# Optimization experiments

Measured on AMD Instinct MI355X. Metric: run time of the kernel, lower is better.

## Reference

```python
import jax, jax.numpy as jnp
import numpy as np

B, T, I, H, O = 64, 2048, 128, 256, 128


def setup_inputs() -> dict:
    key = jax.random.key(0)
    ks = jax.random.split(key, 7)
    s_xh = 1.0 / np.sqrt(I)
    s_hh = 1.0 / np.sqrt(H)
    return {
        "x": jax.random.normal(ks[0], (B, T, I), dtype=jnp.float32),
        "h0": jax.random.normal(ks[1], (B, H), dtype=jnp.float32),
        "Wxh": jax.random.uniform(ks[2], (H, I), jnp.float32, -s_xh, s_xh),
        "Whh": jax.random.uniform(ks[3], (H, H), jnp.float32, -s_hh, s_hh),
        "bh": jax.random.uniform(ks[4], (H,), jnp.float32, -s_hh, s_hh),
        "Wout": jax.random.uniform(ks[5], (O, H), jnp.float32, -s_hh, s_hh),
        "bout": jax.random.uniform(ks[6], (O,), jnp.float32, -s_hh, s_hh),
    }


def reference(x, h0, Wxh, Whh, bh, Wout, bout):
    # x: (B, T, I) -> scan over time with hidden state h: (B, H)
    def step(h, xt):
        # Elman cell: h' = tanh(x Wxh^T + h Whh^T + b)
        h_new = jnp.tanh(xt @ Wxh.T + h @ Whh.T + bh)
        y = h_new @ Wout.T + bout  # (B, O) per-step output head
        return h_new, y

    xT = jnp.swapaxes(x, 0, 1)  # (T, B, I)
    hT, Ys = jax.lax.scan(step, h0, xT)
    Y = jnp.swapaxes(Ys, 0, 1)  # (B, T, O)
    return Y, hT
```

## Files before the change

kernel.cpp:

```cpp
#include <hip/hip_runtime.h>
#include <hip/hip_bf16.h>
#include <hip/hip_fp16.h>

#define B_SZ 64
#define T_SZ 2048
#define I_SZ 128
#define H_SZ 256
#define O_SZ 128

typedef _Float16 half_t;
typedef _Float16 h2_t __attribute__((ext_vector_type(2)));
typedef __fp16   fp16x2_t __attribute__((ext_vector_type(2)));
typedef _Float16 h8_t __attribute__((ext_vector_type(8)));
typedef float    f4_t __attribute__((ext_vector_type(4)));

static __device__ __forceinline__ h2_t uint_as_h2(unsigned u) {
  union { unsigned u; h2_t h; } x; x.u = u; return x.h;
}
static __device__ __forceinline__ unsigned pack_h2(float a, float b) {
#if __has_builtin(__builtin_amdgcn_cvt_pkrtz)
  union { fp16x2_t h; unsigned u; } x;
  x.h = __builtin_amdgcn_cvt_pkrtz(a, b);
  return x.u;
#else
  h2_t h; h[0] = (_Float16)a; h[1] = (_Float16)b;
  union { h2_t h; unsigned u; } x2; x2.h = h; return x2.u;
#endif
}
static __device__ __forceinline__ float dot2(h2_t a, h2_t b, float c) {
#if __has_builtin(__builtin_amdgcn_fdot2)
  return __builtin_amdgcn_fdot2(a, b, c, false);
#else
  return c + (float)a[0] * (float)b[0] + (float)a[1] * (float)b[1];
#endif
}
static __device__ __forceinline__ float fast_rcp(float x) {
#if __has_builtin(__builtin_amdgcn_rcpf)
  return __builtin_amdgcn_rcpf(x);
#else
  return 1.0f / x;
#endif
}

template <int BM, int BN, int BK, int KTOT, bool A_HALF, bool OUT_HALF>
__global__ __launch_bounds__(256, 2) void gemm_tn_bias(
    const void* __restrict__ Ap, const float* __restrict__ Bw,
    const float* __restrict__ bias, void* __restrict__ Out, int ldo) {
  extern __shared__ half_t lds[];
  half_t* As = lds;
  half_t* Bs = lds + BM * BK;

  const int tid = threadIdx.x;
  const long row0 = (long)blockIdx.x * BM;
  const int col0 = blockIdx.y * BN;

  constexpr int MI = 4;
  constexpr int NJ = (BN / 2) / 16;
  const int lane = tid & 63, wid = tid >> 6;
  const int wm = (wid >> 1) * 64;
  const int wn = (wid & 1) * (BN / 2);

  f4_t acc[MI][NJ];
#pragma unroll
  for (int mi = 0; mi < MI; ++mi)
#pragma unroll
    for (int nj = 0; nj < NJ; ++nj) acc[mi][nj] = (f4_t){0.f, 0.f, 0.f, 0.f};

#pragma unroll 1
  for (int kt = 0; kt < KTOT / BK; ++kt) {
    if (kt) __syncthreads();
    constexpr int AIT = (BM * BK) / (256 * 8);
#pragma unroll
    for (int it = 0; it < AIT; ++it) {
      int idx = (it * 256 + tid) * 8;
      int r = idx / BK, c = idx % BK;
      uint4 v;
      if (A_HALF) {
        v = *(const uint4*)((const half_t*)Ap + (row0 + r) * (long)KTOT +
                            kt * BK + c);
      } else {
        const float* src =
            (const float*)Ap + (row0 + r) * (long)KTOT + kt * BK + c;
        float4 f0 = *(const float4*)(src);
        float4 f1 = *(const float4*)(src + 4);
        v.x = pack_h2(f0.x, f0.y); v.y = pack_h2(f0.z, f0.w);
        v.z = pack_h2(f1.x, f1.y); v.w = pack_h2(f1.z, f1.w);
      }
      int chunk = (c >> 3) ^ (r & 7);
      *(uint4*)(&As[r * BK + chunk * 8]) = v;
    }
    constexpr int BIT = (BN * BK) / (256 * 8);
#pragma unroll
    for (int it = 0; it < BIT; ++it) {
      int idx = (it * 256 + tid) * 8;
      int r = idx / BK, c = idx % BK;
      const float* src = Bw + (long)(col0 + r) * KTOT + kt * BK + c;
      float4 f0 = *(const float4*)(src);
      float4 f1 = *(const float4*)(src + 4);
      uint4 v;
      v.x = pack_h2(f0.x, f0.y); v.y = pack_h2(f0.z, f0.w);
      v.z = pack_h2(f1.x, f1.y); v.w = pack_h2(f1.z, f1.w);
      int chunk = (c >> 3) ^ (r & 7);
      *(uint4*)(&Bs[r * BK + chunk * 8]) = v;
    }
    __syncthreads();

#pragma unroll
    for (int ks = 0; ks < BK / 32; ++ks) {
      h8_t af[MI], bf[NJ];
#pragma unroll
      for (int mi = 0; mi < MI; ++mi) {
        int r = wm + mi * 16 + (lane & 15);
        int chunk = (ks * 4 + (lane >> 4)) ^ (r & 7);
        af[mi] = *(const h8_t*)(&As[r * BK + chunk * 8]);
      }
#pragma unroll
      for (int nj = 0; nj < NJ; ++nj) {
        int r = wn + nj * 16 + (lane & 15);
        int chunk = (ks * 4 + (lane >> 4)) ^ (r & 7);
        bf[nj] = *(const h8_t*)(&Bs[r * BK + chunk * 8]);
      }
#pragma unroll
      for (int mi = 0; mi < MI; ++mi)
#pragma unroll
        for (int nj = 0; nj < NJ; ++nj)
          acc[mi][nj] = __builtin_amdgcn_mfma_f32_16x16x32_f16(
              af[mi], bf[nj], acc[mi][nj], 0, 0, 0);
    }
  }

#pragma unroll
  for (int mi = 0; mi < MI; ++mi) {
#pragma unroll
    for (int nj = 0; nj < NJ; ++nj) {
#pragma unroll
      for (int e = 0; e < 4; ++e) {
        long row = row0 + wm + mi * 16 + (lane >> 4) * 4 + e;
        int col = col0 + wn + nj * 16 + (lane & 15);
        float val = acc[mi][nj][e] + bias[col];
        if (OUT_HALF)
          ((half_t*)Out)[row * ldo + col] = (half_t)val;
        else
          ((float*)Out)[row * ldo + col] = val;
      }
    }
  }
}

__global__ __launch_bounds__(512, 1) void rnn_scan(
    const half_t* __restrict__ Xp,
    const float* __restrict__ Whh,
    const float* __restrict__ h0,
    half_t* __restrict__ Hs,
    float* __restrict__ hT) {
  __shared__ __align__(16) unsigned short hbuf[2][H_SZ];
  const int tid = threadIdx.x;
  const int b = blockIdx.x;
  const int lane = tid & 63;
  const int w = tid >> 6;
  const int out = w * 32 + (lane & 31);
  const int kh = lane >> 5;

  unsigned wpk[64];
  {
    const float* wrow = Whh + out * H_SZ + kh * 128;
#pragma unroll
    for (int i = 0; i < 32; ++i) {
      float4 f = *(const float4*)(wrow + i * 4);
      wpk[2 * i] = pack_h2(f.x, f.y);
      wpk[2 * i + 1] = pack_h2(f.z, f.w);
    }
  }
  if (tid < H_SZ) {
    union { _Float16 h; unsigned short s; } cv;
    cv.h = (_Float16)h0[b * H_SZ + tid];
    hbuf[0][tid] = cv.s;
  }
  __syncthreads();

  const half_t* xp = Xp + (long)b * T_SZ * H_SZ + out;
  half_t* hs = Hs + (long)b * T_SZ * H_SZ + out;
  const bool writer = (kh == 0);

  half_t xv = xp[0];
#pragma unroll 1
  for (int t = 0; t < T_SZ; ++t) {
    half_t xnxt = (t + 1 < T_SZ) ? xp[(long)(t + 1) * H_SZ] : (half_t)0.0f;
    const int cur = t & 1;
    const uint4* hp = (const uint4*)(&hbuf[cur][kh * 128]);
    float a0 = 0.f, a1 = 0.f, a2 = 0.f, a3 = 0.f;
#pragma unroll
    for (int i = 0; i < 16; ++i) {
      uint4 v = hp[i];
      a0 = dot2(uint_as_h2(wpk[4 * i + 0]), uint_as_h2(v.x), a0);
      a1 = dot2(uint_as_h2(wpk[4 * i + 1]), uint_as_h2(v.y), a1);
      a2 = dot2(uint_as_h2(wpk[4 * i + 2]), uint_as_h2(v.z), a2);
      a3 = dot2(uint_as_h2(wpk[4 * i + 3]), uint_as_h2(v.w), a3);
    }
    float a = (a0 + a1) + (a2 + a3);
    a += __shfl_xor(a, 32);
    a += (float)xv;
    float ex = __expf(2.0f * a);
    float hn = 1.0f - 2.0f * fast_rcp(ex + 1.0f);

    if (writer) {
      union { _Float16 h; unsigned short s; } cv;
      cv.h = (_Float16)hn;
      hs[(long)t * H_SZ] = cv.h;
      hbuf[cur ^ 1][out] = cv.s;
      if (t == T_SZ - 1) hT[b * H_SZ + out] = hn;
    }
    xv = xnxt;
    __syncthreads();
  }
}

extern "C" void kernel_launch(void* const* d_in, const int* in_sizes, int n_in,
                              void* d_out, int out_size, void* d_ws,
                              size_t ws_size, hipStream_t stream) {
  const float* x = (const float*)d_in[0];
  const float* h0 = (const float*)d_in[1];
  const float* Wxh = (const float*)d_in[2];
  const float* Whh = (const float*)d_in[3];
  const float* bh = (const float*)d_in[4];
  const float* Wout = (const float*)d_in[5];
  const float* bout = (const float*)d_in[6];

  half_t* Xp = (half_t*)d_out;
  half_t* Hs = (half_t*)d_ws;
  float* Y = (float*)d_out;
  float* hT = (float*)d_out + (long)B_SZ * T_SZ * O_SZ;

  const long M = (long)B_SZ * T_SZ;

  {
    dim3 grid((unsigned)(M / 128), H_SZ / 128);
    size_t sh = 2ull * 128 * 128 * sizeof(half_t);
    hipLaunchKernelGGL((gemm_tn_bias<128, 128, 128, 128, false, true>), grid,
                       dim3(256), sh, stream, (const void*)x, Wxh, bh,
                       (void*)Xp, H_SZ);
  }
  hipLaunchKernelGGL(rnn_scan, dim3(B_SZ), dim3(512), 0, stream, Xp, Whh, h0,
                     Hs, hT);
  {
    dim3 grid((unsigned)(M / 128), O_SZ / 128);
    size_t sh = 2ull * 128 * 128 * sizeof(half_t);
    hipLaunchKernelGGL((gemm_tn_bias<128, 128, 128, 256, true, false>), grid,
                       dim3(256), sh, stream, (const void*)Hs, Wout, bout,
                       (void*)Y, O_SZ);
  }
}
```

Before: 1.318 ms.

## Batch 16 RNN chains per block and compute recurrence with MFMA

Rewrites the sequential scan so each block handles 16 batch chains and computes the hidden-state update h·Whh^T with 16x16x32 f16 MFMA instructions instead of per-thread dot2 reductions. Whh fragments live in registers, the hidden state is double-buffered in swizzled LDS, and the x-projection loads are prefetched four steps ahead. This amortizes the per-step barrier and latency across 16 chains but leaves only 4 blocks on the GPU, so the serial step latency (MFMA plus LDS plus sync) now bounds the runtime.

```diff
diff --git a/kernel.cpp b/kernel.cpp
--- a/kernel.cpp
+++ b/kernel.cpp
@@ -7,12 +7,14 @@
 #define I_SZ 128
 #define H_SZ 256
 #define O_SZ 128
+#define CH   16
 
 typedef _Float16 half_t;
 typedef _Float16 h2_t __attribute__((ext_vector_type(2)));
 typedef __fp16   fp16x2_t __attribute__((ext_vector_type(2)));
 typedef _Float16 h8_t __attribute__((ext_vector_type(8)));
 typedef float    f4_t __attribute__((ext_vector_type(4)));
+typedef unsigned int u2_t __attribute__((ext_vector_type(2)));
 
 static __device__ __forceinline__ h2_t uint_as_h2(unsigned u) {
   union { unsigned u; h2_t h; } x; x.u = u; return x.h;
@@ -27,19 +29,16 @@
   union { h2_t h; unsigned u; } x2; x2.h = h; return x2.u;
 #endif
 }
-static __device__ __forceinline__ float dot2(h2_t a, h2_t b, float c) {
-#if __has_builtin(__builtin_amdgcn_fdot2)
-  return __builtin_amdgcn_fdot2(a, b, c, false);
-#else
-  return c + (float)a[0] * (float)b[0] + (float)a[1] * (float)b[1];
-#endif
-}
 static __device__ __forceinline__ float fast_rcp(float x) {
 #if __has_builtin(__builtin_amdgcn_rcpf)
   return __builtin_amdgcn_rcpf(x);
 #else
   return 1.0f / x;
 #endif
+}
+static __device__ __forceinline__ float tanh_fast(float z) {
+  float ex = __expf(2.0f * z);
+  return 1.0f - 2.0f * fast_rcp(ex + 1.0f);
 }
 
 template <int BM, int BN, int BK, int KTOT, bool A_HALF, bool OUT_HALF>
@@ -147,71 +146,120 @@
   }
 }
 
-__global__ __launch_bounds__(512, 1) void rnn_scan(
+__global__ __launch_bounds__(512, 1) void rnn_scan_mfma(
     const half_t* __restrict__ Xp,
     const float* __restrict__ Whh,
     const float* __restrict__ h0,
     half_t* __restrict__ Hs,
     float* __restrict__ hT) {
-  __shared__ __align__(16) unsigned short hbuf[2][H_SZ];
+  __shared__ __align__(16) unsigned char hl[2][CH * 512];
   const int tid = threadIdx.x;
-  const int b = blockIdx.x;
+  const int b0 = blockIdx.x * CH;
   const int lane = tid & 63;
   const int w = tid >> 6;
-  const int out = w * 32 + (lane & 31);
-  const int kh = lane >> 5;
-
-  unsigned wpk[64];
+  const int chain = lane & 15;
+  const int hi = lane >> 4;
+  const int swz = (chain & 7) << 4;
+
+  h8_t wfrag[2][8];
+#pragma unroll
+  for (int mt2 = 0; mt2 < 2; ++mt2) {
+    const int row = (2 * w + mt2) * 16 + chain;
+#pragma unroll
+    for (int ks = 0; ks < 8; ++ks) {
+      const float* p = Whh + row * H_SZ + ks * 32 + hi * 8;
+      float4 f0 = *(const float4*)(p);
+      float4 f1 = *(const float4*)(p + 4);
+      union { unsigned u[4]; h8_t h; } cv;
+      cv.u[0] = pack_h2(f0.x, f0.y); cv.u[1] = pack_h2(f0.z, f0.w);
+      cv.u[2] = pack_h2(f1.x, f1.y); cv.u[3] = pack_h2(f1.z, f1.w);
+      wfrag[mt2][ks] = cv.h;
+    }
+  }
   {
-    const float* wrow = Whh + out * H_SZ + kh * 128;
-#pragma unroll
-    for (int i = 0; i < 32; ++i) {
-      float4 f = *(const float4*)(wrow + i * 4);
-      wpk[2 * i] = pack_h2(f.x, f.y);
-      wpk[2 * i + 1] = pack_h2(f.z, f.w);
-    }
-  }
-  if (tid < H_SZ) {
-    union { _Float16 h; unsigned short s; } cv;
-    cv.h = (_Float16)h0[b * H_SZ + tid];
-    hbuf[0][tid] = cv.s;
+    const int c = tid >> 5;
+    const int col = (tid & 31) * 8;
+    const float* p = h0 + (long)(b0 + c) * H_SZ + col;
+    float4 f0 = *(const float4*)(p);
+    float4 f1 = *(const float4*)(p + 4);
+    uint4 v;
+    v.x = pack_h2(f0.x, f0.y); v.y = pack_h2(f0.z, f0.w);
+    v.z = pack_h2(f1.x, f1.y); v.w = pack_h2(f1.z, f1.w);
+    *(uint4*)&hl[0][(c * 512 + col * 2) ^ ((c & 7) << 4)] = v;
   }
   __syncthreads();
 
-  const half_t* xp = Xp + (long)b * T_SZ * H_SZ + out;
-  half_t* hs = Hs + (long)b * T_SZ * H_SZ + out;
-  const bool writer = (kh == 0);
-
-  half_t xv = xp[0];
+  const int n0[2] = {(2 * w) * 16 + hi * 4, (2 * w + 1) * 16 + hi * 4};
+  const half_t* xb = Xp + (long)(b0 + chain) * T_SZ * H_SZ;
+  half_t* hsb = Hs + (long)(b0 + chain) * T_SZ * H_SZ;
+  float* hTb = hT + (long)(b0 + chain) * H_SZ;
+
+  u2_t xcur[4][2], xnxt[4][2];
+#pragma unroll
+  for (int j = 0; j < 4; ++j) {
+    xcur[j][0] = *(const u2_t*)(xb + (long)j * H_SZ + n0[0]);
+    xcur[j][1] = *(const u2_t*)(xb + (long)j * H_SZ + n0[1]);
+  }
+
 #pragma unroll 1
-  for (int t = 0; t < T_SZ; ++t) {
-    half_t xnxt = (t + 1 < T_SZ) ? xp[(long)(t + 1) * H_SZ] : (half_t)0.0f;
-    const int cur = t & 1;
-    const uint4* hp = (const uint4*)(&hbuf[cur][kh * 128]);
-    float a0 = 0.f, a1 = 0.f, a2 = 0.f, a3 = 0.f;
-#pragma unroll
-    for (int i = 0; i < 16; ++i) {
-      uint4 v = hp[i];
-      a0 = dot2(uint_as_h2(wpk[4 * i + 0]), uint_as_h2(v.x), a0);
-      a1 = dot2(uint_as_h2(wpk[4 * i + 1]), uint_as_h2(v.y), a1);
-      a2 = dot2(uint_as_h2(wpk[4 * i + 2]), uint_as_h2(v.z), a2);
-      a3 = dot2(uint_as_h2(wpk[4 * i + 3]), uint_as_h2(v.w), a3);
-    }
-    float a = (a0 + a1) + (a2 + a3);
-    a += __shfl_xor(a, 32);
-    a += (float)xv;
-    float ex = __expf(2.0f * a);
-    float hn = 1.0f - 2.0f * fast_rcp(ex + 1.0f);
-
-    if (writer) {
-      union { _Float16 h; unsigned short s; } cv;
-      cv.h = (_Float16)hn;
-      hs[(long)t * H_SZ] = cv.h;
-      hbuf[cur ^ 1][out] = cv.s;
-      if (t == T_SZ - 1) hT[b * H_SZ + out] = hn;
-    }
-    xv = xnxt;
-    __syncthreads();
+  for (int tc = 0; tc < T_SZ; tc += 4) {
+#pragma unroll
+    for (int j = 0; j < 4; ++j) {
+      long tt = tc + 4 + j;
+      if (tt > T_SZ - 1) tt = T_SZ - 1;
+      xnxt[j][0] = *(const u2_t*)(xb + tt * H_SZ + n0[0]);
+      xnxt[j][1] = *(const u2_t*)(xb + tt * H_SZ + n0[1]);
+    }
+#pragma unroll
+    for (int j = 0; j < 4; ++j) {
+      const int t = tc + j;
+      const int cur = t & 1;
+      h8_t hf[8];
+#pragma unroll
+      for (int ks = 0; ks < 8; ++ks)
+        hf[ks] =
+            *(const h8_t*)&hl[cur][(chain * 512 + ks * 64 + hi * 16) ^ swz];
+      f4_t a0[2], a1[2];
+#pragma unroll
+      for (int mt2 = 0; mt2 < 2; ++mt2) {
+        a0[mt2] = (f4_t){0.f, 0.f, 0.f, 0.f};
+        a1[mt2] = (f4_t){0.f, 0.f, 0.f, 0.f};
+#pragma unroll
+        for (int ks = 0; ks < 8; ks += 2) {
+          a0[mt2] = __builtin_amdgcn_mfma_f32_16x16x32_f16(
+              wfrag[mt2][ks], hf[ks], a0[mt2], 0, 0, 0);
+          a1[mt2] = __builtin_amdgcn_mfma_f32_16x16x32_f16(
+              wfrag[mt2][ks + 1], hf[ks + 1], a1[mt2], 0, 0, 0);
+        }
+      }
+#pragma unroll
+      for (int mt2 = 0; mt2 < 2; ++mt2) {
+        f4_t acc = a0[mt2] + a1[mt2];
+        h2_t xlo = uint_as_h2(xcur[j][mt2][0]);
+        h2_t xhi = uint_as_h2(xcur[j][mt2][1]);
+        float v0 = tanh_fast(acc[0] + (float)xlo[0]);
+        float v1 = tanh_fast(acc[1] + (float)xlo[1]);
+        float v2 = tanh_fast(acc[2] + (float)xhi[0]);
+        float v3 = tanh_fast(acc[3] + (float)xhi[1]);
+        u2_t pk;
+        pk[0] = pack_h2(v0, v1);
+        pk[1] = pack_h2(v2, v3);
+        const int woff =
+            (chain * 512 + ((2 * w + mt2) * 16 + hi * 4) * 2) ^ swz;
+        *(u2_t*)&hl[cur ^ 1][woff] = pk;
+        *(u2_t*)(hsb + (long)t * H_SZ + n0[mt2]) = pk;
+        if (t == T_SZ - 1) {
+          float4 fo = {v0, v1, v2, v3};
+          *(float4*)(hTb + n0[mt2]) = fo;
+        }
+      }
+      __syncthreads();
+    }
+#pragma unroll
+    for (int j = 0; j < 4; ++j) {
+      xcur[j][0] = xnxt[j][0];
+      xcur[j][1] = xnxt[j][1];
+    }
   }
 }
 
@@ -240,8 +288,8 @@
                        dim3(256), sh, stream, (const void*)x, Wxh, bh,
                        (void*)Xp, H_SZ);
   }
-  hipLaunchKernelGGL(rnn_scan, dim3(B_SZ), dim3(512), 0, stream, Xp, Whh, h0,
-                     Hs, hT);
+  hipLaunchKernelGGL(rnn_scan_mfma, dim3(B_SZ / CH), dim3(512), 0, stream, Xp,
+                     Whh, h0, Hs, hT);
   {
     dim3 grid((unsigned)(M / 128), O_SZ / 128);
     size_t sh = 2ull * 128 * 128 * sizeof(half_t);
```

Result: slower. 2.069 ms (+57.0%).
